# Kernel tuning notes

Hardware: AMD Instinct MI355X
Metric: run time of the kernel (lower is better)

## Reference

```python
import jax, jax.numpy as jnp
import numpy as np

B, S, E, HID, NTR, NCAL, CW, VOCAB, POS = 4096, 201, 32, 512, 4, 8, 16, 32, 256
LN_EPS = 1e-5


def _ln(x, g, b):
    m = x.mean(-1, keepdims=True)
    v = ((x - m) ** 2).mean(-1, keepdims=True)
    return (x - m) * jax.lax.rsqrt(v + LN_EPS) * g + b


def setup_inputs() -> dict:
    key = jax.random.key(0)
    ks = jax.random.split(key, 24)
    g = lambda i, shape, s=0.1: (jax.random.normal(ks[i], shape, jnp.float32) * s)
    return dict(
        encoded_seq=jax.random.randint(ks[0], (B, S), 0, VOCAB, jnp.int32),
        experiment_id=jax.random.randint(ks[1], (B,), 0, NCAL, jnp.int32),
        tok_emb=g(2, (VOCAB, E), 1.0),
        pos_emb=g(3, (POS, E), 1.0),
        ln1_g=jnp.ones((NTR, E)), ln1_b=jnp.zeros((NTR, E)),
        wq=g(4, (NTR, E, E)), wk=g(5, (NTR, E, E)), wv=g(6, (NTR, E, E)),
        bq=g(7, (NTR, E), 0.01), bk=g(8, (NTR, E), 0.01), bv=g(9, (NTR, E), 0.01),
        wo=g(10, (NTR, E, E)), bo=g(11, (NTR, E), 0.01),
        ln2_g=jnp.ones((NTR, E)), ln2_b=jnp.zeros((NTR, E)),
        w1=g(12, (NTR, E, HID)), b1=g(13, (NTR, HID), 0.01),
        w2=g(14, (NTR, HID, E)), b2=g(15, (NTR, E), 0.01),
        lnf_g=jnp.ones((E,)), lnf_b=jnp.zeros((E,)),
        wpen=g(16, (E, 1)), bpen=g(17, (1,), 0.01),
        wfan=g(18, (1, CW)), bfan=g(19, (CW,), 0.01),
        wcal=g(20, (NCAL, CW, 1)), bcal=g(21, (NCAL, 1), 0.01),
    )


def reference(encoded_seq, experiment_id, tok_emb, pos_emb,
              ln1_g, ln1_b, wq, wk, wv, bq, bk, bv, wo, bo,
              ln2_g, ln2_b, w1, b1, w2, b2,
              lnf_g, lnf_b, wpen, bpen, wfan, bfan, wcal, bcal):
    # embedding + positional add: [B,S,E]
    x = tok_emb[encoded_seq] + pos_emb[jnp.arange(S)]
    scale = 1.0 / jnp.sqrt(jnp.float32(E))  # num_heads=1 => head_dim=E
    for i in range(NTR):
        n = _ln(x, ln1_g[i], ln1_b[i])
        q = n @ wq[i] + bq[i]
        k = n @ wk[i] + bk[i]
        v = n @ wv[i] + bv[i]
        a = jax.nn.softmax(jnp.einsum('bqe,bke->bqk', q, k) * scale, axis=-1)
        att = jnp.einsum('bqk,bke->bqe', a, v) @ wo[i] + bo[i]
        x = x + att
        h = _ln(x, ln2_g[i], ln2_b[i])
        x = x + (jax.nn.silu(h @ w1[i] + b1[i]) @ w2[i] + b2[i])
    contrib = _ln(x, lnf_g, lnf_b) @ wpen + bpen        # [B,S,1]
    underlying = contrib.sum(axis=-2)                    # [B,1]
    pre = jax.nn.elu(underlying @ wfan + bfan)           # [B,CW]
    # all calibrator heads at once: [B,NCAL]
    all_corr = jnp.einsum('bc,ncj->bn', pre, wcal) + bcal[:, 0]
    mask = jax.nn.one_hot(experiment_id, NCAL, dtype=pre.dtype)  # exactly the (exp==id) mask-sum
    corrected = (all_corr * mask).sum(-1, keepdims=True) + underlying
    return corrected.squeeze()
```

## Files before the change

### kernel.cpp

```cpp
#include <hip/hip_runtime.h>


#define SS   201
#define SP   208
#define NMT  13
#define EE   32
#define HIDN 512
#define NTRL 4
#define CWN  16
#define BB   4096
#define XST  36
#define VWST 228

#define X_OFF    0
#define K_OFF    14976
#define VWT_OFF  29952
#define MS_OFF   44544
#define RS_OFF   45376
#define BIAS_OFF 46208
#define SMEM_SZ  47232

#define WS_FRAG  0
#define WS_BIAS  294912
#define WS_B1    299008
#define WS_FIN   307200
#define L2E      1.4426950408889634f

typedef unsigned short u16;
typedef unsigned int   u32;
typedef short bf16x4 __attribute__((ext_vector_type(4)));
typedef short bf16x8 __attribute__((ext_vector_type(8)));
typedef float f32x4  __attribute__((ext_vector_type(4)));
typedef float f32x2  __attribute__((ext_vector_type(2)));

__device__ __forceinline__ f32x4 MF(bf16x8 a, bf16x8 b, f32x4 c){
  return __builtin_amdgcn_mfma_f32_16x16x32_bf16(a, b, c, 0, 0, 0);
}
__device__ __forceinline__ float bf2f(u16 u){ return __uint_as_float(((u32)u)<<16); }
__device__ __forceinline__ u16 f2bf(float f){
  u32 u = __float_as_uint(f);
  u += 0x7fffu + ((u>>16)&1u);
  return (u16)(u>>16);
}
__device__ __forceinline__ u32 pk2bf(f32x2 v){
#if defined(__has_builtin) && __has_builtin(__builtin_amdgcn_cvt_pk_bf16_f32)
  auto r = __builtin_amdgcn_cvt_pk_bf16_f32(v.x, v.y);
  u32 u; __builtin_memcpy(&u, &r, 4); return u;
#else
  return ((__float_as_uint(v.x)+0x8000u)>>16) | ((__float_as_uint(v.y)+0x8000u) & 0xffff0000u);
#endif
}
__device__ __forceinline__ f32x2 upk2(u32 d){
  return f32x2{ __uint_as_float(d<<16), __uint_as_float(d & 0xffff0000u) };
}
template<bool F32>
__device__ __forceinline__ float ldv(const void* p, int i){
  if (F32) return ((const float*)p)[i];
  return bf2f(((const u16*)p)[i]);
}
template<bool F32>
__device__ __forceinline__ u16 ldbf(const void* p, int i){
  if (F32) return f2bf(((const float*)p)[i]);
  return ((const u16*)p)[i];
}
__device__ __forceinline__ bf16x8 cat44(bf16x4 lo, bf16x4 hi){
  bf16x8 r = {lo[0],lo[1],lo[2],lo[3],hi[0],hi[1],hi[2],hi[3]};
  return r;
}
__device__ __forceinline__ bf16x8 mk8(u32 a0, u32 a1, u32 a2, u32 a3){
  u32 t[4] = {a0,a1,a2,a3};
  bf16x8 r; __builtin_memcpy(&r, t, 16); return r;
}
__device__ __forceinline__ u32 spk(f32x2 z){
  const f32x2 nl2e2 = {-L2E, -L2E};
  const f32x2 one2  = {1.f, 1.f};
  f32x2 a = z * nl2e2;
  f32x2 e = { __builtin_amdgcn_exp2f(a.x), __builtin_amdgcn_exp2f(a.y) };
  f32x2 d = one2 + e;
  f32x2 rc = { __builtin_amdgcn_rcpf(d.x), __builtin_amdgcn_rcpf(d.y) };
  f32x2 s = z * rc;
  return pk2bf(s);
}

__device__ __forceinline__ int sniff_bf16(const void* tok_emb, int tid){
  int sane = 0;
  if (tid < 64){
    u16 wd = ((const u16*)tok_emb)[tid];
    int e = (wd >> 7) & 0xFF;
    sane = (e >= 100 && e <= 140) ? 1 : 0;
  }
  return (__syncthreads_count(sane) >= 52) ? 1 : 0;
}

template<bool F32>
__device__ __forceinline__ void frag_body(const void* wq, const void* wk,
    const void* wv, const void* wo, const void* w1, const void* w2, void* ws)
{
  int t = blockIdx.x;
  int l = t / 72, k = t % 72;
  int lane = threadIdx.x, l16 = lane & 15, quad = lane >> 4;
  bf16x8 v;
  if (k < 8){
    int mat = k >> 1, half = k & 1;
    if (mat == 2){
      int col = half*16 + l16;
      #pragma unroll
      for (int j=0;j<8;j++){
        int a = quad*8 + j;
        float acc = 0.f;
        for (int e=0;e<EE;e++)
          acc += ldv<F32>(wv, l*1024 + a*32 + e) * ldv<F32>(wo, l*1024 + e*32 + col);
        v[j] = (short)f2bf(acc);
      }
    } else {
      const void* src = (mat==0)? wq : (mat==1)? wk : wo;
      #pragma unroll
      for (int j=0;j<8;j++)
        v[j] = (short)ldbf<F32>(src, l*1024 + (quad*8+j)*32 + half*16 + l16);
    }
  } else if (k < 40){
    int nt = k - 8;
    #pragma unroll
    for (int j=0;j<8;j++)
      v[j] = (short)ldbf<F32>(w1, l*16384 + (quad*8+j)*512 + nt*16 + l16);
  } else {
    int kc = (k-40)>>1, nh = (k-40)&1;
    #pragma unroll
    for (int j=0;j<8;j++){
      int hh = kc*32 + ((j&4) ? 16 : 0) + quad*4 + (j&3);
      v[j] = (short)ldbf<F32>(w2, l*16384 + hh*32 + nh*16 + l16);
    }
  }
  *(bf16x8*)((char*)ws + WS_FRAG + t*1024 + lane*16) = v;
}

__global__ __launch_bounds__(64) void fmt_frags(
    const void* __restrict__ tok_emb,
    const void* __restrict__ wq, const void* __restrict__ wk,
    const void* __restrict__ wv, const void* __restrict__ wo,
    const void* __restrict__ w1, const void* __restrict__ w2,
    void* __restrict__ ws)
{
  if (sniff_bf16(tok_emb, threadIdx.x)) frag_body<false>(wq,wk,wv,wo,w1,w2,ws);
  else                                  frag_body<true >(wq,wk,wv,wo,w1,w2,ws);
}

template<bool F32>
__device__ __forceinline__ void bias_body(
    const void* bq, const void* bk, const void* bv, const void* wo, const void* bo,
    const void* ln1_g, const void* ln1_b, const void* ln2_g, const void* ln2_b,
    const void* b1, const void* b2,
    const void* lnf_g, const void* lnf_b, const void* wpen, const void* bpen,
    const void* wfan, const void* bfan, const void* wcal, const void* bcal,
    void* ws)
{
  int tid = threadIdx.x, idx = tid & 31, grp = tid >> 5;
  float* BW  = (float*)((char*)ws + WS_BIAS);
  float* BW1 = (float*)((char*)ws + WS_B1);
  float* FW  = (float*)((char*)ws + WS_FIN);
  for (int l=0;l<NTRL;l++){
    float v = 0.f;
    switch(grp){
      case 0: v = ldv<F32>(bq, l*32+idx); break;
      case 1: v = ldv<F32>(bk, l*32+idx); break;
      case 2: {
        float acc = ldv<F32>(bo, l*32+idx);
        for (int e=0;e<EE;e++) acc += ldv<F32>(bv, l*32+e) * ldv<F32>(wo, l*1024 + e*32 + idx);
        v = acc; break;
      }
      case 3: v = ldv<F32>(ln1_g, l*32+idx); break;
      case 4: v = ldv<F32>(ln1_b, l*32+idx); break;
      case 5: v = ldv<F32>(ln2_g, l*32+idx); break;
      case 6: v = ldv<F32>(ln2_b, l*32+idx); break;
      case 7: v = ldv<F32>(b2,   l*32+idx); break;
    }
    BW[l*256 + tid] = v;
  }
  for (int i=tid; i<NTRL*HIDN; i+=256) BW1[i] = ldv<F32>(b1, i);
  if (tid < 32){
    FW[tid]    = ldv<F32>(lnf_g, tid);
    FW[32+tid] = ldv<F32>(lnf_b, tid);
    FW[64+tid] = ldv<F32>(wpen, tid);
  }
  if (tid == 0) FW[96] = ldv<F32>(bpen, 0);
  if (tid < 16){ FW[97+tid] = ldv<F32>(wfan, tid); FW[113+tid] = ldv<F32>(bfan, tid); }
  if (tid < 128) FW[129+tid] = ldv<F32>(wcal, tid);
  if (tid < 8)   FW[257+tid] = ldv<F32>(bcal, tid);
}

__global__ __launch_bounds__(256) void fmt_bias(
    const void* __restrict__ tok_emb,
    const void* __restrict__ bq, const void* __restrict__ bk,
    const void* __restrict__ bv, const void* __restrict__ wo, const void* __restrict__ bo,
    const void* __restrict__ ln1_g, const void* __restrict__ ln1_b,
    const void* __restrict__ ln2_g, const void* __restrict__ ln2_b,
    const void* __restrict__ b1, const void* __restrict__ b2,
    const void* __restrict__ lnf_g, const void* __restrict__ lnf_b,
    const void* __restrict__ wpen, const void* __restrict__ bpen,
    const void* __restrict__ wfan, const void* __restrict__ bfan,
    const void* __restrict__ wcal, const void* __restrict__ bcal,
    void* __restrict__ ws)
{
  if (sniff_bf16(tok_emb, threadIdx.x))
    bias_body<false>(bq,bk,bv,wo,bo,ln1_g,ln1_b,ln2_g,ln2_b,b1,b2,
                     lnf_g,lnf_b,wpen,bpen,wfan,bfan,wcal,bcal,ws);
  else
    bias_body<true >(bq,bk,bv,wo,bo,ln1_g,ln1_b,ln2_g,ln2_b,b1,b2,
                     lnf_g,lnf_b,wpen,bpen,wfan,bfan,wcal,bcal,ws);
}

__device__ __forceinline__ void ln_stats(const u16* Xb, float* MS, float* RS, int tid){
  if (tid < SP){
    const u32* row = (const u32*)(Xb + tid*XST);
    f32x2 s2 = {0.f,0.f}, q2 = {0.f,0.f};
    #pragma unroll
    for (int i=0;i<16;i++){ f32x2 p = upk2(row[i]); s2 += p; q2 += p*p; }
    float m = (s2.x + s2.y) * (1.f/EE);
    float v = (q2.x + q2.y) * (1.f/EE) - m*m;
    MS[tid] = m;
    RS[tid] = rsqrtf(v + 1e-5f);
  }
}

__device__ __forceinline__ bf16x8 build_nfrag(const u16* Xb, const float* MS, const float* RS,
                                              int row, int quad, const f32x2* G2, const f32x2* B2){
  const u32* raw = (const u32*)(Xb + row*XST + quad*8);
  f32x2 m2 = { MS[row], MS[row] };
  f32x2 rs2 = { RS[row], RS[row] };
  u32 o[4];
  #pragma unroll
  for (int p=0;p<4;p++){
    f32x2 x = upk2(raw[p]);
    o[p] = pk2bf((x - m2) * rs2 * G2[p] + B2[p]);
  }
  bf16x8 r; __builtin_memcpy(&r, o, 16);
  return r;
}

template<bool F32>
__device__ __forceinline__ void tr_body(
    const int* seq, const int* expid,
    const void* tok_emb, const void* pos_emb,
    const void* ws, void* out, unsigned char* smem)
{
  u16*   Xb   = (u16*)(smem + X_OFF);
  u16*   Kb   = (u16*)(smem + K_OFF);
  u16*   VWTb = (u16*)(smem + VWT_OFF);
  float* MS   = (float*)(smem + MS_OFF);
  float* RS   = (float*)(smem + RS_OFF);
  float* BIAS = (float*)(smem + BIAS_OFF);

  const int tid  = threadIdx.x;
  const int lane = tid & 63, w = tid >> 6;
  const int l16  = lane & 15, quad = lane >> 4;
  const int b    = blockIdx.x;
  const f32x4 Z  = {0.f,0.f,0.f,0.f};

  {
    const int* srow = seq + b*SS;
    for (int i = tid; i < SP*EE; i += 256){
      int s = i >> 5, e = i & 31;
      float val = 0.f;
      if (s < SS){
        int tok = srow[s];
        val = ldv<F32>(tok_emb, tok*EE + e) + ldv<F32>(pos_emb, s*EE + e);
      }
      Xb[s*XST + e] = f2bf(val);
    }
  }
  __syncthreads();

  const float qce = 0.2550546813f;
  const f32x2 qce2 = {qce, qce};

  for (int l = 0; l < NTRL; ++l){
    const char* wsl = (const char*)ws + WS_FRAG + l*73728;
    bf16x8 bwq0 = *(const bf16x8*)(wsl + 0*1024 + lane*16);
    bf16x8 bwq1 = *(const bf16x8*)(wsl + 1*1024 + lane*16);
    bf16x8 bwk0 = *(const bf16x8*)(wsl + 2*1024 + lane*16);
    bf16x8 bwk1 = *(const bf16x8*)(wsl + 3*1024 + lane*16);
    bf16x8 bwv0 = *(const bf16x8*)(wsl + 4*1024 + lane*16);
    bf16x8 bwv1 = *(const bf16x8*)(wsl + 5*1024 + lane*16);
    {
      const float* BW = (const float*)((const char*)ws + WS_BIAS) + l*256;
      BIAS[tid] = BW[tid];
    }
    ln_stats(Xb, MS, RS, tid);
    __syncthreads();

    bf16x8 aq[4];
    {
      f32x2 G2[4], B2[4];
      #pragma unroll
      for (int p=0;p<4;p++){
        G2[p] = f32x2{BIAS[96+quad*8+2*p], BIAS[96+quad*8+2*p+1]};
        B2[p] = f32x2{BIAS[128+quad*8+2*p], BIAS[128+quad*8+2*p+1]};
      }
      f32x4 bq0 = *(const f32x4*)(BIAS + quad*4);
      f32x4 bq1 = *(const f32x4*)(BIAS + 16 + quad*4);
      float bk0s = BIAS[32+l16], bk1s = BIAS[48+l16];
      f32x4 kc0 = {bk0s,bk0s,bk0s,bk0s};
      f32x4 kc1 = {bk1s,bk1s,bk1s,bk1s};
      #pragma unroll
      for (int t=0;t<4;t++){
        int m = w + 4*t;
        if (m < NMT){
          int m16 = m*16;
          bf16x8 an = build_nfrag(Xb, MS, RS, m16+l16, quad, G2, B2);
          f32x4 ck0 = MF(an, bwk0, kc0), ck1 = MF(an, bwk1, kc1);
          #pragma unroll
          for (int r=0;r<4;r++){
            int row = m16 + quad*4 + r;
            u32 pk = pk2bf(f32x2{ck0[r], ck1[r]});
            Kb[row*XST + l16]      = (u16)pk;
            Kb[row*XST + 16 + l16] = (u16)(pk>>16);
          }
          f32x4 cw0 = MF(an, bwv0, Z), cw1 = MF(an, bwv1, Z);
          #pragma unroll
          for (int r=0;r<4;r++){
            u32 pk = pk2bf(f32x2{cw0[r], cw1[r]});
            VWTb[l16*VWST      + m16 + quad*4 + r] = (u16)pk;
            VWTb[(16+l16)*VWST + m16 + quad*4 + r] = (u16)(pk>>16);
          }
          f32x4 cq0 = MF(bwq0, an, bq0), cq1 = MF(bwq1, an, bq1);
          aq[t] = mk8(pk2bf(f32x2{cq0[0],cq0[1]}*qce2), pk2bf(f32x2{cq0[2],cq0[3]}*qce2),
                      pk2bf(f32x2{cq1[0],cq1[1]}*qce2), pk2bf(f32x2{cq1[2],cq1[3]}*qce2));
        }
      }
    }
    __syncthreads();

    {
      const u16* vbase0 = VWTb + l16*VWST;
      const u16* vbase1 = VWTb + (16+l16)*VWST;
      f32x4 ob0 = *(const f32x4*)(BIAS + 64 + quad*4);
      f32x4 ob1 = *(const f32x4*)(BIAS + 80 + quad*4);
      #pragma unroll
      for (int t=0;t<4;t++){
        int m = w + 4*t;
        if (m < NMT){
          int m16 = m*16;
          u32 pbw[13][2];
          f32x2 pacc = {0.f, 0.f};
          #pragma unroll
          for (int kt=0; kt<13; kt++){
            const u16* krow = Kb + (kt*16+l16)*XST;
            bf16x8 kb8 = cat44(*(const bf16x4*)(krow + quad*4),
                               *(const bf16x4*)(krow + 16 + quad*4));
            f32x4 St = MF(kb8, aq[t], Z);
            f32x2 ea = { __builtin_amdgcn_exp2f(St[0]), __builtin_amdgcn_exp2f(St[1]) };
            f32x2 eb = { __builtin_amdgcn_exp2f(St[2]), __builtin_amdgcn_exp2f(St[3]) };
            if (kt == 12){
              int kb = quad*4;
              if (kb+0 >= 9) ea.x = 0.f;
              if (kb+1 >= 9) ea.y = 0.f;
              if (kb+2 >= 9) eb.x = 0.f;
              if (kb+3 >= 9) eb.y = 0.f;
            }
            pacc += ea + eb;
            pbw[kt][0] = pk2bf(ea);
            pbw[kt][1] = pk2bf(eb);
          }
          float part = pacc.x + pacc.y;
          part += __shfl_xor(part, 16);
          part += __shfl_xor(part, 32);
          float inv = __builtin_amdgcn_rcpf(part);

          f32x4 o0 = Z, o1 = Z;
          #pragma unroll
          for (int c=0;c<6;c++){
            bf16x4 a0l = *(const bf16x4*)(vbase0 + c*32 + quad*4);
            bf16x4 a0h = *(const bf16x4*)(vbase0 + c*32 + 16 + quad*4);
            bf16x4 a1l = *(const bf16x4*)(vbase1 + c*32 + quad*4);
            bf16x4 a1h = *(const bf16x4*)(vbase1 + c*32 + 16 + quad*4);
            bf16x8 B8 = mk8(pbw[2*c][0], pbw[2*c][1], pbw[2*c+1][0], pbw[2*c+1][1]);
            o0 = MF(cat44(a0l, a0h), B8, o0);
            o1 = MF(cat44(a1l, a1h), B8, o1);
          }
          {
            bf16x4 a0l = *(const bf16x4*)(vbase0 + 192 + quad*4);
            bf16x4 a1l = *(const bf16x4*)(vbase1 + 192 + quad*4);
            bf16x8 B8 = mk8(pbw[12][0], pbw[12][1], 0u, 0u);
            o0 = MF(cat44(a0l, a0l), B8, o0);
            o1 = MF(cat44(a1l, a1l), B8, o1);
          }

          u32* xr = (u32*)(Xb + (m16+l16)*XST);
          {
            u32 d0 = xr[quad*2], d1 = xr[quad*2+1];
            f32x2 r01 = f32x2{o0[0],o0[1]} * inv + (upk2(d0) + f32x2{ob0[0],ob0[1]});
            f32x2 r23 = f32x2{o0[2],o0[3]} * inv + (upk2(d1) + f32x2{ob0[2],ob0[3]});
            xr[quad*2]   = pk2bf(r01);
            xr[quad*2+1] = pk2bf(r23);
            u32 d2 = xr[8+quad*2], d3 = xr[8+quad*2+1];
            f32x2 s01 = f32x2{o1[0],o1[1]} * inv + (upk2(d2) + f32x2{ob1[0],ob1[1]});
            f32x2 s23 = f32x2{o1[2],o1[3]} * inv + (upk2(d3) + f32x2{ob1[2],ob1[3]});
            xr[8+quad*2]   = pk2bf(s01);
            xr[8+quad*2+1] = pk2bf(s23);
          }
        }
      }
    }
    __syncthreads();

    ln_stats(Xb, MS, RS, tid);
    __syncthreads();

    {
      f32x2 G2[4], B2[4];
      #pragma unroll
      for (int p=0;p<4;p++){
        G2[p] = f32x2{BIAS[160+quad*8+2*p], BIAS[160+quad*8+2*p+1]};
        B2[p] = f32x2{BIAS[192+quad*8+2*p], BIAS[192+quad*8+2*p+1]};
      }
      bf16x8 anc[4];
      #pragma unroll
      for (int t=0;t<4;t++){
        int m = w + 4*t;
        if (m < NMT) anc[t] = build_nfrag(Xb, MS, RS, m*16+l16, quad, G2, B2);
      }
      f32x4 oacc[4][2];
      #pragma unroll
      for (int t=0;t<4;t++){ oacc[t][0] = Z; oacc[t][1] = Z; }
      const char* w1f = wsl + 8*1024;
      const char* w2f = wsl + 40*1024;
      const float* BW1 = (const float*)((const char*)ws + WS_B1) + l*HIDN;

      for (int hp = 0; hp < 16; ++hp){
        bf16x8 a1lo = *(const bf16x8*)(w1f + (2*hp  )*1024 + lane*16);
        bf16x8 a1hi = *(const bf16x8*)(w1f + (2*hp+1)*1024 + lane*16);
        bf16x8 a2e0 = *(const bf16x8*)(w2f + (hp*2  )*1024 + lane*16);
        bf16x8 a2e1 = *(const bf16x8*)(w2f + (hp*2+1)*1024 + lane*16);
        f32x4 b1q0 = *(const f32x4*)(BW1 + hp*32      + quad*4);
        f32x4 b1q1 = *(const f32x4*)(BW1 + hp*32 + 16 + quad*4);
        #pragma unroll
        for (int t=0;t<4;t++){
          int m = w + 4*t;
          if (m < NMT){
            f32x4 z0 = MF(a1lo, anc[t], b1q0);
            f32x4 z1 = MF(a1hi, anc[t], b1q1);
            bf16x8 H8 = mk8(spk(f32x2{z0[0], z0[1]}), spk(f32x2{z0[2], z0[3]}),
                            spk(f32x2{z1[0], z1[1]}), spk(f32x2{z1[2], z1[3]}));
            oacc[t][0] = MF(a2e0, H8, oacc[t][0]);
            oacc[t][1] = MF(a2e1, H8, oacc[t][1]);
          }
        }
      }

      f32x4 b2q0 = *(const f32x4*)(BIAS + 224 + quad*4);
      f32x4 b2q1 = *(const f32x4*)(BIAS + 240 + quad*4);
      #pragma unroll
      for (int t=0;t<4;t++){
        int m = w + 4*t;
        if (m < NMT){
          u32* xr = (u32*)(Xb + (m*16 + l16)*XST);
          u32 d0 = xr[quad*2], d1 = xr[quad*2+1];
          f32x2 r01 = f32x2{oacc[t][0][0], oacc[t][0][1]} + (upk2(d0) + f32x2{b2q0[0], b2q0[1]});
          f32x2 r23 = f32x2{oacc[t][0][2], oacc[t][0][3]} + (upk2(d1) + f32x2{b2q0[2], b2q0[3]});
          xr[quad*2]   = pk2bf(r01);
          xr[quad*2+1] = pk2bf(r23);
          u32 d2 = xr[8+quad*2], d3 = xr[8+quad*2+1];
          f32x2 s01 = f32x2{oacc[t][1][0], oacc[t][1][1]} + (upk2(d2) + f32x2{b2q1[0], b2q1[1]});
          f32x2 s23 = f32x2{oacc[t][1][2], oacc[t][1][3]} + (upk2(d3) + f32x2{b2q1[2], b2q1[3]});
          xr[8+quad*2]   = pk2bf(s01);
          xr[8+quad*2+1] = pk2bf(s23);
        }
      }
    }
    __syncthreads();
  }

  const float* FW = (const float*)((const char*)ws + WS_FIN);
  if (tid < 32){
    BIAS[tid]    = FW[tid];
    BIAS[32+tid] = FW[32+tid];
    BIAS[64+tid] = FW[64+tid];
  }
  __syncthreads();
  float part = 0.f;
  if (tid < SS){
    const u32* row = (const u32*)(Xb + tid*XST);
    f32x2 v[16]; f32x2 s2 = {0.f,0.f};
    #pragma unroll
    for (int i=0;i<16;i++){ f32x2 p = upk2(row[i]); v[i] = p; s2 += p; }
    float m = (s2.x+s2.y) * (1.f/EE);
    f32x2 m2 = {m,m};
    f32x2 var2 = {0.f,0.f};
    #pragma unroll
    for (int i=0;i<16;i++){ f32x2 d = v[i]-m2; var2 += d*d; }
    float rs = rsqrtf((var2.x+var2.y)*(1.f/EE) + 1e-5f);
    f32x2 rs2 = {rs, rs};
    f32x2 dot2 = {0.f,0.f};
    #pragma unroll
    for (int i=0;i<16;i++){
      f32x2 g  = {BIAS[2*i], BIAS[2*i+1]};
      f32x2 bb = {BIAS[32+2*i], BIAS[33+2*i]};
      f32x2 wp = {BIAS[64+2*i], BIAS[65+2*i]};
      dot2 += ((v[i]-m2)*rs2*g + bb) * wp;
    }
    part = dot2.x + dot2.y + FW[96];
  }
  #pragma unroll
  for (int off=32; off; off>>=1) part += __shfl_xor(part, off);
  float* REDF = (float*)(smem + MS_OFF);
  __syncthreads();
  if (lane == 0) REDF[w] = part;
  __syncthreads();
  if (tid == 0){
    float u = REDF[0] + REDF[1] + REDF[2] + REDF[3];
    int ex = expid[b];
    float corr = FW[257+ex];
    #pragma unroll
    for (int c = 0; c < CWN; ++c){
      float pre = u * FW[97+c] + FW[113+c];
      pre = pre > 0.f ? pre : (__expf(pre) - 1.f);
      corr += pre * FW[129 + ex*CWN + c];
    }
    float res = corr + u;
    if (F32) ((float*)out)[b] = res;
    else     ((u16*)out)[b]  = f2bf(res);
  }
}

__global__ __launch_bounds__(256, 3) void tr_kernel(
    const int* __restrict__ seq, const int* __restrict__ expid,
    const void* __restrict__ tok_emb, const void* __restrict__ pos_emb,
    const void* __restrict__ ws, void* __restrict__ out)
{
  __shared__ __align__(16) unsigned char smem[SMEM_SZ];
  if (sniff_bf16(tok_emb, threadIdx.x))
    tr_body<false>(seq, expid, tok_emb, pos_emb, ws, out, smem);
  else
    tr_body<true >(seq, expid, tok_emb, pos_emb, ws, out, smem);
}

extern "C" void kernel_launch(void* const* d_in, const int* in_sizes, int n_in,
                              void* d_out, int out_size, void* d_ws, size_t ws_size,
                              hipStream_t stream)
{
  (void)in_sizes; (void)n_in; (void)ws_size; (void)out_size;
  const void* tok_emb = d_in[2];
  fmt_frags<<<dim3(288), dim3(64), 0, stream>>>(
      tok_emb, d_in[6], d_in[7], d_in[8], d_in[12], d_in[16], d_in[18], d_ws);
  fmt_bias<<<dim3(1), dim3(256), 0, stream>>>(
      tok_emb, d_in[9], d_in[10], d_in[11], d_in[12], d_in[13],
      d_in[4], d_in[5], d_in[14], d_in[15], d_in[17], d_in[19],
      d_in[20], d_in[21], d_in[22], d_in[23],
      d_in[24], d_in[25], d_in[26], d_in[27], d_ws);
  tr_kernel<<<dim3(BB), dim3(256), 0, stream>>>(
      (const int*)d_in[0], (const int*)d_in[1], tok_emb, d_in[3], d_ws, d_out);
}
```

Measured before the change: 882.0 us.

## Compute LayerNorm stats in registers, drop shared bias staging and syncs

LayerNorm mean and rstd are now computed per wave from the MFMA row fragments with cross-lane shuffles, fused into the residual-update epilogues. This removes the shared MS/RS/BIAS arrays and several block barriers per layer, and biases are read straight from global memory. The K and V·Wo staging layouts are repacked so each score and PV fragment comes from a single 16-byte load instead of two 8-byte halves, and the query scale is folded into Wq and bq during preprocessing. Shared memory drops, so launch bounds move to 4 blocks per CU. The trade-offs are higher register pressure under the tighter bound and one less barrier at the end of each layer, which relies on each wave touching only its own rows.

```diff
diff --git a/kernel.cpp b/kernel.cpp
--- a/kernel.cpp
+++ b/kernel.cpp
@@ -9,22 +9,19 @@
 #define NTRL 4
 #define CWN  16
 #define BB   4096
-#define XST  36
-#define VWST 228
+#define XST  32
 
 #define X_OFF    0
-#define K_OFF    14976
-#define VWT_OFF  29952
-#define MS_OFF   44544
-#define RS_OFF   45376
-#define BIAS_OFF 46208
-#define SMEM_SZ  47232
+#define K2_OFF   13312
+#define VW2_OFF  26624
+#define SMEM_SZ  39936
 
 #define WS_FRAG  0
 #define WS_BIAS  294912
 #define WS_B1    299008
 #define WS_FIN   307200
 #define L2E      1.4426950408889634f
+#define QCE      0.2550546813f
 
 typedef unsigned short u16;
 typedef unsigned int   u32;
@@ -63,13 +60,13 @@
   if (F32) return f2bf(((const float*)p)[i]);
   return ((const u16*)p)[i];
 }
-__device__ __forceinline__ bf16x8 cat44(bf16x4 lo, bf16x4 hi){
-  bf16x8 r = {lo[0],lo[1],lo[2],lo[3],hi[0],hi[1],hi[2],hi[3]};
-  return r;
-}
 __device__ __forceinline__ bf16x8 mk8(u32 a0, u32 a1, u32 a2, u32 a3){
   u32 t[4] = {a0,a1,a2,a3};
   bf16x8 r; __builtin_memcpy(&r, t, 16); return r;
+}
+__device__ __forceinline__ bf16x8 dup8(bf16x4 v){
+  bf16x8 r = {v[0],v[0],v[1],v[1],v[2],v[2],v[3],v[3]};
+  return r;
 }
 __device__ __forceinline__ u32 spk(f32x2 z){
   const f32x2 nl2e2 = {-L2E, -L2E};
@@ -112,8 +109,12 @@
           acc += ldv<F32>(wv, l*1024 + a*32 + e) * ldv<F32>(wo, l*1024 + e*32 + col);
         v[j] = (short)f2bf(acc);
       }
+    } else if (mat == 0){
+      #pragma unroll
+      for (int j=0;j<8;j++)
+        v[j] = (short)f2bf(QCE * ldv<F32>(wq, l*1024 + (quad*8+j)*32 + half*16 + l16));
     } else {
-      const void* src = (mat==0)? wq : (mat==1)? wk : wo;
+      const void* src = (mat==1)? wk : wo;
       #pragma unroll
       for (int j=0;j<8;j++)
         v[j] = (short)ldbf<F32>(src, l*1024 + (quad*8+j)*32 + half*16 + l16);
@@ -161,7 +162,7 @@
   for (int l=0;l<NTRL;l++){
     float v = 0.f;
     switch(grp){
-      case 0: v = ldv<F32>(bq, l*32+idx); break;
+      case 0: v = QCE * ldv<F32>(bq, l*32+idx); break;
       case 1: v = ldv<F32>(bk, l*32+idx); break;
       case 2: {
         float acc = ldv<F32>(bo, l*32+idx);
@@ -209,24 +210,11 @@
                      lnf_g,lnf_b,wpen,bpen,wfan,bfan,wcal,bcal,ws);
 }
 
-__device__ __forceinline__ void ln_stats(const u16* Xb, float* MS, float* RS, int tid){
-  if (tid < SP){
-    const u32* row = (const u32*)(Xb + tid*XST);
-    f32x2 s2 = {0.f,0.f}, q2 = {0.f,0.f};
-    #pragma unroll
-    for (int i=0;i<16;i++){ f32x2 p = upk2(row[i]); s2 += p; q2 += p*p; }
-    float m = (s2.x + s2.y) * (1.f/EE);
-    float v = (q2.x + q2.y) * (1.f/EE) - m*m;
-    MS[tid] = m;
-    RS[tid] = rsqrtf(v + 1e-5f);
-  }
-}
-
-__device__ __forceinline__ bf16x8 build_nfrag(const u16* Xb, const float* MS, const float* RS,
-                                              int row, int quad, const f32x2* G2, const f32x2* B2){
+__device__ __forceinline__ bf16x8 nfrag_reg(const u16* Xb, int row, int quad,
+                                            float m, float rs,
+                                            const f32x2* G2, const f32x2* B2){
   const u32* raw = (const u32*)(Xb + row*XST + quad*8);
-  f32x2 m2 = { MS[row], MS[row] };
-  f32x2 rs2 = { RS[row], RS[row] };
+  f32x2 m2 = {m, m}, rs2 = {rs, rs};
   u32 o[4];
   #pragma unroll
   for (int p=0;p<4;p++){
@@ -237,19 +225,22 @@
   return r;
 }
 
+__device__ __forceinline__ void red_stats(float ps, float pq, float& m, float& rs){
+  ps += __shfl_xor(ps, 16); ps += __shfl_xor(ps, 32);
+  pq += __shfl_xor(pq, 16); pq += __shfl_xor(pq, 32);
+  m  = ps * (1.f/EE);
+  rs = rsqrtf(pq * (1.f/EE) - m*m + 1e-5f);
+}
+
 template<bool F32>
 __device__ __forceinline__ void tr_body(
     const int* seq, const int* expid,
     const void* tok_emb, const void* pos_emb,
     const void* ws, void* out, unsigned char* smem)
 {
-  u16*   Xb   = (u16*)(smem + X_OFF);
-  u16*   Kb   = (u16*)(smem + K_OFF);
-  u16*   VWTb = (u16*)(smem + VWT_OFF);
-  float* MS   = (float*)(smem + MS_OFF);
-  float* RS   = (float*)(smem + RS_OFF);
-  float* BIAS = (float*)(smem + BIAS_OFF);
-
+  u16* Xb  = (u16*)(smem + X_OFF);
+  u32* K2  = (u32*)(smem + K2_OFF);
+  u16* VW2 = (u16*)(smem + VW2_OFF);
   const int tid  = threadIdx.x;
   const int lane = tid & 63, w = tid >> 6;
   const int l16  = lane & 15, quad = lane >> 4;
@@ -270,35 +261,40 @@
   }
   __syncthreads();
 
-  const float qce = 0.2550546813f;
-  const f32x2 qce2 = {qce, qce};
+  float m1[4], rs1[4], m2v[4], rs2v[4];
+  #pragma unroll
+  for (int t=0;t<4;t++){
+    int m = w + 4*t;
+    if (m < NMT){
+      const u32* raw = (const u32*)(Xb + (m*16+l16)*XST + quad*8);
+      f32x2 s2 = {0.f,0.f}, q2 = {0.f,0.f};
+      #pragma unroll
+      for (int p=0;p<4;p++){ f32x2 x = upk2(raw[p]); s2 += x; q2 += x*x; }
+      red_stats(s2.x+s2.y, q2.x+q2.y, m1[t], rs1[t]);
+    }
+  }
 
   for (int l = 0; l < NTRL; ++l){
     const char* wsl = (const char*)ws + WS_FRAG + l*73728;
+    const float* BW = (const float*)((const char*)ws + WS_BIAS) + l*256;
     bf16x8 bwq0 = *(const bf16x8*)(wsl + 0*1024 + lane*16);
     bf16x8 bwq1 = *(const bf16x8*)(wsl + 1*1024 + lane*16);
     bf16x8 bwk0 = *(const bf16x8*)(wsl + 2*1024 + lane*16);
     bf16x8 bwk1 = *(const bf16x8*)(wsl + 3*1024 + lane*16);
     bf16x8 bwv0 = *(const bf16x8*)(wsl + 4*1024 + lane*16);
     bf16x8 bwv1 = *(const bf16x8*)(wsl + 5*1024 + lane*16);
-    {
-      const float* BW = (const float*)((const char*)ws + WS_BIAS) + l*256;
-      BIAS[tid] = BW[tid];
-    }
-    ln_stats(Xb, MS, RS, tid);
-    __syncthreads();
 
     bf16x8 aq[4];
     {
       f32x2 G2[4], B2[4];
       #pragma unroll
       for (int p=0;p<4;p++){
-        G2[p] = f32x2{BIAS[96+quad*8+2*p], BIAS[96+quad*8+2*p+1]};
-        B2[p] = f32x2{BIAS[128+quad*8+2*p], BIAS[128+quad*8+2*p+1]};
-      }
-      f32x4 bq0 = *(const f32x4*)(BIAS + quad*4);
-      f32x4 bq1 = *(const f32x4*)(BIAS + 16 + quad*4);
-      float bk0s = BIAS[32+l16], bk1s = BIAS[48+l16];
+        G2[p] = f32x2{BW[96+quad*8+2*p],  BW[96+quad*8+2*p+1]};
+        B2[p] = f32x2{BW[128+quad*8+2*p], BW[128+quad*8+2*p+1]};
+      }
+      f32x4 bq0 = *(const f32x4*)(BW + quad*4);
+      f32x4 bq1 = *(const f32x4*)(BW + 16 + quad*4);
+      float bk0s = BW[32+l16], bk1s = BW[48+l16];
       f32x4 kc0 = {bk0s,bk0s,bk0s,bk0s};
       f32x4 kc1 = {bk1s,bk1s,bk1s,bk1s};
       #pragma unroll
@@ -306,60 +302,79 @@
         int m = w + 4*t;
         if (m < NMT){
           int m16 = m*16;
-          bf16x8 an = build_nfrag(Xb, MS, RS, m16+l16, quad, G2, B2);
+          bf16x8 an = nfrag_reg(Xb, m16+l16, quad, m1[t], rs1[t], G2, B2);
           f32x4 ck0 = MF(an, bwk0, kc0), ck1 = MF(an, bwk1, kc1);
           #pragma unroll
-          for (int r=0;r<4;r++){
-            int row = m16 + quad*4 + r;
-            u32 pk = pk2bf(f32x2{ck0[r], ck1[r]});
-            Kb[row*XST + l16]      = (u16)pk;
-            Kb[row*XST + 16 + l16] = (u16)(pk>>16);
-          }
+          for (int r=0;r<4;r++)
+            K2[(m16 + quad*4 + r)*16 + l16] = pk2bf(f32x2{ck0[r], ck1[r]});
           f32x4 cw0 = MF(an, bwv0, Z), cw1 = MF(an, bwv1, Z);
-          #pragma unroll
-          for (int r=0;r<4;r++){
-            u32 pk = pk2bf(f32x2{cw0[r], cw1[r]});
-            VWTb[l16*VWST      + m16 + quad*4 + r] = (u16)pk;
-            VWTb[(16+l16)*VWST + m16 + quad*4 + r] = (u16)(pk>>16);
+          if (m == 12){
+            #pragma unroll
+            for (int r=0;r<4;r++){
+              u32 pk = pk2bf(f32x2{cw0[r], cw1[r]});
+              VW2[l16*208      + 192 + quad*4 + r] = (u16)pk;
+              VW2[(16+l16)*208 + 192 + quad*4 + r] = (u16)(pk>>16);
+            }
+          } else {
+            #pragma unroll
+            for (int r=0;r<4;r++){
+              u32 pk = pk2bf(f32x2{cw0[r], cw1[r]});
+              int colu = ((m>>1)*16 + quad*4 + r)*2 + (m&1);
+              VW2[l16*208      + colu] = (u16)pk;
+              VW2[(16+l16)*208 + colu] = (u16)(pk>>16);
+            }
           }
           f32x4 cq0 = MF(bwq0, an, bq0), cq1 = MF(bwq1, an, bq1);
-          aq[t] = mk8(pk2bf(f32x2{cq0[0],cq0[1]}*qce2), pk2bf(f32x2{cq0[2],cq0[3]}*qce2),
-                      pk2bf(f32x2{cq1[0],cq1[1]}*qce2), pk2bf(f32x2{cq1[2],cq1[3]}*qce2));
+          aq[t] = mk8(pk2bf(f32x2{cq0[0],cq1[0]}), pk2bf(f32x2{cq0[1],cq1[1]}),
+                      pk2bf(f32x2{cq0[2],cq1[2]}), pk2bf(f32x2{cq0[3],cq1[3]}));
         }
       }
     }
     __syncthreads();
 
     {
-      const u16* vbase0 = VWTb + l16*VWST;
-      const u16* vbase1 = VWTb + (16+l16)*VWST;
-      f32x4 ob0 = *(const f32x4*)(BIAS + 64 + quad*4);
-      f32x4 ob1 = *(const f32x4*)(BIAS + 80 + quad*4);
+      const u32* vb0 = (const u32*)VW2 + l16*104;
+      const u32* vb1 = (const u32*)VW2 + (16+l16)*104;
+      f32x4 ob0 = *(const f32x4*)(BW + 64 + quad*4);
+      f32x4 ob1 = *(const f32x4*)(BW + 80 + quad*4);
       #pragma unroll
       for (int t=0;t<4;t++){
         int m = w + 4*t;
         if (m < NMT){
           int m16 = m*16;
-          u32 pbw[13][2];
+          u32 pbw[7][4];
           f32x2 pacc = {0.f, 0.f};
           #pragma unroll
-          for (int kt=0; kt<13; kt++){
-            const u16* krow = Kb + (kt*16+l16)*XST;
-            bf16x8 kb8 = cat44(*(const bf16x4*)(krow + quad*4),
-                               *(const bf16x4*)(krow + 16 + quad*4));
-            f32x4 St = MF(kb8, aq[t], Z);
-            f32x2 ea = { __builtin_amdgcn_exp2f(St[0]), __builtin_amdgcn_exp2f(St[1]) };
-            f32x2 eb = { __builtin_amdgcn_exp2f(St[2]), __builtin_amdgcn_exp2f(St[3]) };
-            if (kt == 12){
-              int kb = quad*4;
-              if (kb+0 >= 9) ea.x = 0.f;
-              if (kb+1 >= 9) ea.y = 0.f;
-              if (kb+2 >= 9) eb.x = 0.f;
-              if (kb+3 >= 9) eb.y = 0.f;
-            }
-            pacc += ea + eb;
-            pbw[kt][0] = pk2bf(ea);
-            pbw[kt][1] = pk2bf(eb);
+          for (int c=0;c<6;c++){
+            const bf16x8 ka = *(const bf16x8*)(K2 + ((2*c  )*16+l16)*16 + quad*4);
+            const bf16x8 kb = *(const bf16x8*)(K2 + ((2*c+1)*16+l16)*16 + quad*4);
+            f32x4 S0 = MF(ka, aq[t], Z);
+            f32x4 S1 = MF(kb, aq[t], Z);
+            f32x2 ea0 = { __builtin_amdgcn_exp2f(S0[0]), __builtin_amdgcn_exp2f(S0[1]) };
+            f32x2 eb0 = { __builtin_amdgcn_exp2f(S0[2]), __builtin_amdgcn_exp2f(S0[3]) };
+            f32x2 ea1 = { __builtin_amdgcn_exp2f(S1[0]), __builtin_amdgcn_exp2f(S1[1]) };
+            f32x2 eb1 = { __builtin_amdgcn_exp2f(S1[2]), __builtin_amdgcn_exp2f(S1[3]) };
+            pacc += (ea0 + eb0) + (ea1 + eb1);
+            pbw[c][0] = pk2bf(f32x2{ea0.x, ea1.x});
+            pbw[c][1] = pk2bf(f32x2{ea0.y, ea1.y});
+            pbw[c][2] = pk2bf(f32x2{eb0.x, eb1.x});
+            pbw[c][3] = pk2bf(f32x2{eb0.y, eb1.y});
+          }
+          {
+            const bf16x8 ka = *(const bf16x8*)(K2 + (12*16+l16)*16 + quad*4);
+            f32x4 S0 = MF(ka, aq[t], Z);
+            f32x2 ea0 = { __builtin_amdgcn_exp2f(S0[0]), __builtin_amdgcn_exp2f(S0[1]) };
+            f32x2 eb0 = { __builtin_amdgcn_exp2f(S0[2]), __builtin_amdgcn_exp2f(S0[3]) };
+            int kb_ = quad*4;
+            if (kb_+0 >= 9) ea0.x = 0.f;
+            if (kb_+1 >= 9) ea0.y = 0.f;
+            if (kb_+2 >= 9) eb0.x = 0.f;
+            if (kb_+3 >= 9) eb0.y = 0.f;
+            pacc += ea0 + eb0;
+            pbw[6][0] = pk2bf(f32x2{ea0.x, 0.f});
+            pbw[6][1] = pk2bf(f32x2{ea0.y, 0.f});
+            pbw[6][2] = pk2bf(f32x2{eb0.x, 0.f});
+            pbw[6][3] = pk2bf(f32x2{eb0.y, 0.f});
           }
           float part = pacc.x + pacc.y;
           part += __shfl_xor(part, 16);
@@ -369,55 +384,51 @@
           f32x4 o0 = Z, o1 = Z;
           #pragma unroll
           for (int c=0;c<6;c++){
-            bf16x4 a0l = *(const bf16x4*)(vbase0 + c*32 + quad*4);
-            bf16x4 a0h = *(const bf16x4*)(vbase0 + c*32 + 16 + quad*4);
-            bf16x4 a1l = *(const bf16x4*)(vbase1 + c*32 + quad*4);
-            bf16x4 a1h = *(const bf16x4*)(vbase1 + c*32 + 16 + quad*4);
-            bf16x8 B8 = mk8(pbw[2*c][0], pbw[2*c][1], pbw[2*c+1][0], pbw[2*c+1][1]);
-            o0 = MF(cat44(a0l, a0h), B8, o0);
-            o1 = MF(cat44(a1l, a1h), B8, o1);
+            bf16x8 A0 = *(const bf16x8*)(vb0 + c*16 + quad*4);
+            bf16x8 A1 = *(const bf16x8*)(vb1 + c*16 + quad*4);
+            bf16x8 B8 = mk8(pbw[c][0], pbw[c][1], pbw[c][2], pbw[c][3]);
+            o0 = MF(A0, B8, o0);
+            o1 = MF(A1, B8, o1);
           }
           {
-            bf16x4 a0l = *(const bf16x4*)(vbase0 + 192 + quad*4);
-            bf16x4 a1l = *(const bf16x4*)(vbase1 + 192 + quad*4);
-            bf16x8 B8 = mk8(pbw[12][0], pbw[12][1], 0u, 0u);
-            o0 = MF(cat44(a0l, a0l), B8, o0);
-            o1 = MF(cat44(a1l, a1l), B8, o1);
+            bf16x4 a0l = *(const bf16x4*)((const u16*)vb0 + 192 + quad*4);
+            bf16x4 a1l = *(const bf16x4*)((const u16*)vb1 + 192 + quad*4);
+            bf16x8 B8 = mk8(pbw[6][0], pbw[6][1], pbw[6][2], pbw[6][3]);
+            o0 = MF(dup8(a0l), B8, o0);
+            o1 = MF(dup8(a1l), B8, o1);
           }
 
-          u32* xr = (u32*)(Xb + (m16+l16)*XST);
-          {
-            u32 d0 = xr[quad*2], d1 = xr[quad*2+1];
-            f32x2 r01 = f32x2{o0[0],o0[1]} * inv + (upk2(d0) + f32x2{ob0[0],ob0[1]});
-            f32x2 r23 = f32x2{o0[2],o0[3]} * inv + (upk2(d1) + f32x2{ob0[2],ob0[3]});
-            xr[quad*2]   = pk2bf(r01);
-            xr[quad*2+1] = pk2bf(r23);
-            u32 d2 = xr[8+quad*2], d3 = xr[8+quad*2+1];
-            f32x2 s01 = f32x2{o1[0],o1[1]} * inv + (upk2(d2) + f32x2{ob1[0],ob1[1]});
-            f32x2 s23 = f32x2{o1[2],o1[3]} * inv + (upk2(d3) + f32x2{ob1[2],ob1[3]});
-            xr[8+quad*2]   = pk2bf(s01);
-            xr[8+quad*2+1] = pk2bf(s23);
-          }
+          u32* xr = (u32*)Xb + (m16+l16)*(XST/2);
+          u32 d0 = xr[quad*2], d1 = xr[quad*2+1];
+          f32x2 r01 = f32x2{o0[0],o0[1]} * inv + (upk2(d0) + f32x2{ob0[0],ob0[1]});
+          f32x2 r23 = f32x2{o0[2],o0[3]} * inv + (upk2(d1) + f32x2{ob0[2],ob0[3]});
+          xr[quad*2]   = pk2bf(r01);
+          xr[quad*2+1] = pk2bf(r23);
+          u32 d2 = xr[8+quad*2], d3 = xr[8+quad*2+1];
+          f32x2 s01 = f32x2{o1[0],o1[1]} * inv + (upk2(d2) + f32x2{ob1[0],ob1[1]});
+          f32x2 s23 = f32x2{o1[2],o1[3]} * inv + (upk2(d3) + f32x2{ob1[2],ob1[3]});
+          xr[8+quad*2]   = pk2bf(s01);
+          xr[8+quad*2+1] = pk2bf(s23);
+          f32x2 ss = (r01 + r23) + (s01 + s23);
+          f32x2 qq = r01*r01; qq += r23*r23; qq += s01*s01; qq += s23*s23;
+          red_stats(ss.x+ss.y, qq.x+qq.y, m2v[t], rs2v[t]);
         }
       }
     }
-    __syncthreads();
-
-    ln_stats(Xb, MS, RS, tid);
     __syncthreads();
 
     {
       f32x2 G2[4], B2[4];
       #pragma unroll
       for (int p=0;p<4;p++){
-        G2[p] = f32x2{BIAS[160+quad*8+2*p], BIAS[160+quad*8+2*p+1]};
-        B2[p] = f32x2{BIAS[192+quad*8+2*p], BIAS[192+quad*8+2*p+1]};
+        G2[p] = f32x2{BW[160+quad*8+2*p], BW[160+quad*8+2*p+1]};
+        B2[p] = f32x2{BW[192+quad*8+2*p], BW[192+quad*8+2*p+1]};
       }
       bf16x8 anc[4];
       #pragma unroll
       for (int t=0;t<4;t++){
         int m = w + 4*t;
-        if (m < NMT) anc[t] = build_nfrag(Xb, MS, RS, m*16+l16, quad, G2, B2);
+        if (m < NMT) anc[t] = nfrag_reg(Xb, m*16+l16, quad, m2v[t], rs2v[t], G2, B2);
       }
       f32x4 oacc[4][2];
       #pragma unroll
@@ -447,13 +458,13 @@
         }
       }
 
-      f32x4 b2q0 = *(const f32x4*)(BIAS + 224 + quad*4);
-      f32x4 b2q1 = *(const f32x4*)(BIAS + 240 + quad*4);
+      f32x4 b2q0 = *(const f32x4*)(BW + 224 + quad*4);
+      f32x4 b2q1 = *(const f32x4*)(BW + 240 + quad*4);
       #pragma unroll
       for (int t=0;t<4;t++){
         int m = w + 4*t;
         if (m < NMT){
-          u32* xr = (u32*)(Xb + (m*16 + l16)*XST);
+          u32* xr = (u32*)Xb + (m*16 + l16)*(XST/2);
           u32 d0 = xr[quad*2], d1 = xr[quad*2+1];
           f32x2 r01 = f32x2{oacc[t][0][0], oacc[t][0][1]} + (upk2(d0) + f32x2{b2q0[0], b2q0[1]});
           f32x2 r23 = f32x2{oacc[t][0][2], oacc[t][0][3]} + (upk2(d1) + f32x2{b2q0[2], b2q0[3]});
@@ -464,17 +475,22 @@
           f32x2 s23 = f32x2{oacc[t][1][2], oacc[t][1][3]} + (upk2(d3) + f32x2{b2q1[2], b2q1[3]});
           xr[8+quad*2]   = pk2bf(s01);
           xr[8+quad*2+1] = pk2bf(s23);
+          f32x2 ss = (r01 + r23) + (s01 + s23);
+          f32x2 qq = r01*r01; qq += r23*r23; qq += s01*s01; qq += s23*s23;
+          red_stats(ss.x+ss.y, qq.x+qq.y, m1[t], rs1[t]);
         }
       }
-    }
-    __syncthreads();
-  }
+      asm volatile("" ::: "memory");
+    }
+  }
+  __syncthreads();
 
   const float* FW = (const float*)((const char*)ws + WS_FIN);
+  float* HB = (float*)(smem + K2_OFF);
   if (tid < 32){
-    BIAS[tid]    = FW[tid];
-    BIAS[32+tid] = FW[32+tid];
-    BIAS[64+tid] = FW[64+tid];
+    HB[tid]    = FW[tid];
+    HB[32+tid] = FW[32+tid];
+    HB[64+tid] = FW[64+tid];
   }
   __syncthreads();
   float part = 0.f;
@@ -493,16 +509,16 @@
     f32x2 dot2 = {0.f,0.f};
     #pragma unroll
     for (int i=0;i<16;i++){
-      f32x2 g  = {BIAS[2*i], BIAS[2*i+1]};
-      f32x2 bb = {BIAS[32+2*i], BIAS[33+2*i]};
-      f32x2 wp = {BIAS[64+2*i], BIAS[65+2*i]};
+      f32x2 g  = {HB[2*i], HB[2*i+1]};
+      f32x2 bb = {HB[32+2*i], HB[33+2*i]};
+      f32x2 wp = {HB[64+2*i], HB[65+2*i]};
       dot2 += ((v[i]-m2)*rs2*g + bb) * wp;
     }
     part = dot2.x + dot2.y + FW[96];
   }
   #pragma unroll
   for (int off=32; off; off>>=1) part += __shfl_xor(part, off);
-  float* REDF = (float*)(smem + MS_OFF);
+  float* REDF = (float*)(smem + K2_OFF + 1024);
   __syncthreads();
   if (lane == 0) REDF[w] = part;
   __syncthreads();
@@ -522,7 +538,7 @@
   }
 }
 
-__global__ __launch_bounds__(256, 3) void tr_kernel(
+__global__ __launch_bounds__(256, 4) void tr_kernel(
     const int* __restrict__ seq, const int* __restrict__ expid,
     const void* __restrict__ tok_emb, const void* __restrict__ pos_emb,
     const void* __restrict__ ws, void* __restrict__ out)
```

Result: slower. 932.0 us (+5.7%).
